# Kernel tuning notes

Hardware: AMD Instinct MI355X
Metric: run time of the kernel (lower is better)

The kernel has to match this reference:

```python
import jax, jax.numpy as jnp
import numpy as np

N_HEADS = 16


def setup_inputs() -> dict:
    key = jax.random.key(0)
    ks = jax.random.split(key, 5)
    E = 1024
    x = jax.random.normal(ks[0], (2, 2048, E), dtype=jnp.float32)
    s = 1.0 / np.sqrt(E)
    Wq = jax.random.normal(ks[1], (E, E), dtype=jnp.float32) * s
    Wk = jax.random.normal(ks[2], (E, E), dtype=jnp.float32) * s
    Wv = jax.random.normal(ks[3], (E, E), dtype=jnp.float32) * s
    Wo = jax.random.normal(ks[4], (E, E), dtype=jnp.float32) * s
    bo = jnp.zeros((E,), dtype=jnp.float32)
    return {"x": x, "Wq": Wq, "Wk": Wk, "Wv": Wv, "Wo": Wo, "bo": bo}


def reference(x, Wq, Wk, Wv, Wo, bo):
    B, S, E = x.shape
    H = N_HEADS
    D = E // H
    # project and split heads: [B, H, S, D]
    def split_heads(y):
        return y.reshape(B, S, H, D).transpose(0, 2, 1, 3)
    q = split_heads(x @ Wq)
    k = split_heads(x @ Wk)
    v = split_heads(x @ Wv)
    # full score matrix [B, H, S, S]
    scores = jnp.einsum('bhqd,bhkd->bhqk', q, k)
    causal = jnp.triu(jnp.ones((S, S), dtype=bool), k=1)
    scores = jnp.where(causal, -jnp.inf, scores)
    attn = jax.nn.softmax(scores / jnp.sqrt(jnp.float32(D)), axis=-1)
    # dropout rate is 0.0 -> identity
    ctx = jnp.einsum('bhqk,bhkd->bhqd', attn, v)
    ctx = ctx.transpose(0, 2, 1, 3).reshape(B, S, E)
    return ctx @ Wo + bo
```

## Files before the change

kernel.cpp:

```cpp
#include <hip/hip_runtime.h>
#include <stdint.h>


#define N_HEADS 16
#define HD 64
#define SEQ 2048
#define EMB 1024

typedef __attribute__((ext_vector_type(8))) short s16x8;
typedef __attribute__((ext_vector_type(4))) float f32x4;
typedef __attribute__((ext_vector_type(16))) float f32x16;

#define QSCALE 0.18033688f

template <bool B> struct BC { static constexpr bool value = B; };

__device__ __forceinline__ short f2b(float f) {
  union { float f; uint32_t u; } v; v.f = f;
  uint32_t u = v.u;
  u += 0x7fffu + ((u >> 16) & 1u);
  return (short)(u >> 16);
}

__device__ __forceinline__ uint32_t pk2(float a, float b) {
  union { float f; uint32_t u; } x, y; x.f = a; y.f = b;
  return ((x.u + 0x8000u) >> 16) | ((y.u + 0x8000u) & 0xffff0000u);
}

__device__ __forceinline__ float exp2a(float x) {
  float r; asm("v_exp_f32 %0, %1" : "=v"(r) : "v"(x)); return r;
}

__device__ __forceinline__ void gll16(const void* g, void* l) {
  __builtin_amdgcn_global_load_lds((const __attribute__((address_space(1))) void*)g,
                                   (__attribute__((address_space(3))) void*)l, 16, 0, 0);
}

#define SWZ(row, chunk) ((((row) * 8) + ((chunk) ^ ((row) & 7))) * 8)

__global__ __launch_bounds__(256) void k_prep(const float* __restrict__ x,
                                              const float* __restrict__ W0,
                                              const float* __restrict__ W1,
                                              const float* __restrict__ W2,
                                              const float* __restrict__ W3,
                                              short* __restrict__ xb,
                                              short* __restrict__ wt) {
  const int z = blockIdx.x, t = threadIdx.x;
  if (z < 4096) {
    int i = z * 256 + t;
    float4 v = ((const float4*)x)[i];
    short4 o;
    o.x = f2b(v.x); o.y = f2b(v.y); o.z = f2b(v.z); o.w = f2b(v.w);
    ((short4*)xb)[i] = o;
  } else {
    __shared__ float tile[32][33];
    int bz = z - 4096;
    int w = bz >> 10, rem = bz & 1023;
    int bn = (rem & 31) * 32, bk = (rem >> 5) * 32;
    const float* W = w == 0 ? W0 : w == 1 ? W1 : w == 2 ? W2 : W3;
    short* o = wt + (size_t)w * EMB * EMB;
    int tx = t & 31, ty = t >> 5;
    for (int i = ty; i < 32; i += 8)
      tile[i][tx] = W[(size_t)(bk + i) * EMB + bn + tx];
    __syncthreads();
    for (int i = ty; i < 32; i += 8)
      o[(size_t)(bn + i) * EMB + bk + tx] = f2b(tile[tx][i]);
  }
}

template <int MODE>
__global__ __launch_bounds__(256) void k_gemm(const short* __restrict__ A,
                                              const short* __restrict__ BT,
                                              void* __restrict__ outp,
                                              const float* __restrict__ bias) {
  constexpr int MAIN = 4 * 4096;
  constexpr int EPIL = (MODE == 1) ? 0 : 128 * 132;
  constexpr int SMSZ = MAIN > EPIL ? MAIN : EPIL;
  __shared__ alignas(16) short smem[SMSZ];

  const int t = threadIdx.x;
  const int by = blockIdx.y;
  const int m0 = blockIdx.x * 128;
  const short* Bp = BT + (size_t)by * (128 * EMB);
  const int wave = t >> 6, lane = t & 63;
  const int wm = (wave >> 1) * 64, wn = (wave & 1) * 64;
  const int l31 = lane & 31, lh = lane >> 5;

  const int srow = lane >> 2;
  const int soff = ((lane & 3) ^ (srow & 3)) * 8;

  auto stage = [&](int kb, int p) {
    short* as = smem + p * 4096;
    short* bs = smem + 8192 + p * 4096;
#pragma unroll
    for (int i = 0; i < 2; i++) {
      int rb = wave * 32 + i * 16;
      gll16(A + (size_t)(m0 + rb + srow) * EMB + kb + soff, &as[rb * 32]);
      gll16(Bp + (size_t)(rb + srow) * EMB + kb + soff, &bs[rb * 32]);
    }
  };
  auto frd = [&](const short* sb, int row, int kh) -> s16x8 {
    int c = kh * 2 + lh;
    return *(const s16x8*)&sb[row * 32 + ((c ^ (row & 3)) * 8)];
  };

  f32x16 acc[2][2] = {};

  auto kloop = [&](auto SWC) {
    constexpr bool SW = decltype(SWC)::value;
    int pb = 0;
    stage(0, 0);
    for (int kb = 0; kb < EMB; kb += 32) {
      __syncthreads();
      if (kb + 32 < EMB) stage(kb + 32, pb ^ 1);
      const short* as = smem + pb * 4096;
      const short* bs = smem + 8192 + pb * 4096;
      s16x8 af[2][2], bf[2][2];
#pragma unroll
      for (int mt = 0; mt < 2; mt++)
#pragma unroll
        for (int kh = 0; kh < 2; kh++) af[mt][kh] = frd(as, wm + mt * 32 + l31, kh);
#pragma unroll
      for (int nt = 0; nt < 2; nt++)
#pragma unroll
        for (int kh = 0; kh < 2; kh++) bf[nt][kh] = frd(bs, wn + nt * 32 + l31, kh);
#pragma unroll
      for (int mt = 0; mt < 2; mt++)
#pragma unroll
        for (int nt = 0; nt < 2; nt++)
#pragma unroll
          for (int kh = 0; kh < 2; kh++)
            acc[mt][nt] = SW
              ? __builtin_amdgcn_mfma_f32_32x32x16_bf16(bf[nt][kh], af[mt][kh], acc[mt][nt], 0, 0, 0)
              : __builtin_amdgcn_mfma_f32_32x32x16_bf16(af[mt][kh], bf[nt][kh], acc[mt][nt], 0, 0, 0);
      pb ^= 1;
    }
  };

  if (MODE == 1 || by < 16) kloop(BC<true>{});
  else                      kloop(BC<false>{});

  if (MODE == 0) {
    if (by < 16) {
      __syncthreads();
      short* Vls = smem;
      const int wsel = by >> 3;
      const float qs = (wsel == 0) ? QSCALE : 1.0f;
      const int n0l = (by & 7) * 128;
#pragma unroll
      for (int mt = 0; mt < 2; mt++) {
        int mr = wm + mt * 32 + l31;
#pragma unroll
        for (int nt = 0; nt < 2; nt++)
#pragma unroll
          for (int g = 0; g < 4; g++) {
            uint2 w;
            w.x = pk2(acc[mt][nt][4 * g + 0] * qs, acc[mt][nt][4 * g + 1] * qs);
            w.y = pk2(acc[mt][nt][4 * g + 2] * qs, acc[mt][nt][4 * g + 3] * qs);
            *(uint2*)&Vls[mr * 132 + wn + nt * 32 + g * 8 + 4 * lh] = w;
          }
      }
      __syncthreads();
      short* ob = (short*)outp + (size_t)wsel * (4u * 1024 * 1024);
      const int bb = m0 >> 11, ss0 = m0 & (SEQ - 1);
#pragma unroll
      for (int i = 0; i < 8; i++) {
        int mrow = i * 16 + (t >> 4);
        int ncol = (t & 15) * 8;
        int e = n0l + ncol, hh = e >> 6, dd = e & 63;
        *(uint4*)&ob[(((size_t)(bb * N_HEADS + hh) * SEQ) + ss0 + mrow) * 64 + dd] =
            *(const uint4*)&Vls[mrow * 132 + ncol];
      }
    } else {
      __syncthreads();
      short* Vls = smem;
#pragma unroll
      for (int nt = 0; nt < 2; nt++) {
        int nl = wn + nt * 32 + l31;
#pragma unroll
        for (int mt = 0; mt < 2; mt++)
#pragma unroll
          for (int g = 0; g < 4; g++) {
            uint2 w;
            w.x = pk2(acc[mt][nt][4 * g + 0], acc[mt][nt][4 * g + 1]);
            w.y = pk2(acc[mt][nt][4 * g + 2], acc[mt][nt][4 * g + 3]);
            *(uint2*)&Vls[nl * 132 + wm + mt * 32 + g * 8 + 4 * lh] = w;
          }
      }
      __syncthreads();
      short* obv = (short*)outp + (size_t)8 * 1024 * 1024;
      const int n0l = (by & 7) * 128;
      const int bb = m0 >> 11, ss0 = m0 & (SEQ - 1);
#pragma unroll
      for (int i = 0; i < 8; i++) {
        int nl = i * 16 + (t >> 4);
        int mc = (t & 15) * 8;
        int e = n0l + nl, hh = e >> 6, dd = e & 63;
        *(uint4*)&obv[((size_t)((bb * N_HEADS + hh) * HD + dd)) * SEQ + ss0 + mc] =
            *(const uint4*)&Vls[nl * 132 + mc];
      }
    }
  } else {
    float* of = (float*)outp;
    const int n0 = by * 128;
#pragma unroll
    for (int mt = 0; mt < 2; mt++) {
      int mg = m0 + wm + mt * 32 + l31;
#pragma unroll
      for (int nt = 0; nt < 2; nt++)
#pragma unroll
        for (int g = 0; g < 4; g++) {
          int ng = n0 + wn + nt * 32 + g * 8 + 4 * lh;
          f32x4 bv = *(const f32x4*)&bias[ng];
          f32x4 w;
          w[0] = acc[mt][nt][4 * g + 0] + bv[0];
          w[1] = acc[mt][nt][4 * g + 1] + bv[1];
          w[2] = acc[mt][nt][4 * g + 2] + bv[2];
          w[3] = acc[mt][nt][4 * g + 3] + bv[3];
          *(f32x4*)&of[(size_t)mg * EMB + ng] = w;
        }
    }
  }
}

__global__ __launch_bounds__(512) void k_attn(const short* __restrict__ Q,
                                              const short* __restrict__ K,
                                              const short* __restrict__ Vt,
                                              short* __restrict__ ctx) {
  __shared__ alignas(16) short UQP[128 * 72];
  __shared__ alignas(16) short Ks0[64 * 64], Ks1[64 * 64];
  __shared__ alignas(16) short Vs0[64 * 64], Vs1[64 * 64];

  const int t = threadIdx.x, wave = t >> 6, lane = t & 63;
  const int ml = lane & 15, quad = lane >> 4;
  const int bh = blockIdx.x;
  const int qb = 15 - (int)blockIdx.y;
  const size_t base = (size_t)bh * SEQ * HD;
  const int q0 = qb * 128, wq = q0 + wave * 16;

  const int sr = lane >> 3;
  const int sc = ((lane & 7) ^ sr) * 8;

#pragma unroll
  for (int i = 0; i < 2; i++) {
    int r8 = wave * 16 + i * 8;
    gll16(Q + base + (size_t)(q0 + r8 + sr) * HD + sc, &UQP[r8 * 64]);
  }
  auto stageKV = [&](int kt, short* kd, short* vd) {
    const int kbase = kt * 64;
    const int r8 = wave * 8;
    gll16(K + base + (size_t)(kbase + r8 + sr) * HD + sc, &kd[r8 * 64]);
    gll16(Vt + base + (size_t)(r8 + sr) * SEQ + kbase + sc, &vd[r8 * 64]);
  };

  f32x4 cacc[4] = {};
  float li = 0.f;
  short* Pw = &UQP[wave * 16 * 72];

  stageKV(0, Ks0, Vs0);
  __syncthreads();

  s16x8 qf[2];
#pragma unroll
  for (int c = 0; c < 2; c++)
    qf[c] = *(const s16x8*)&UQP[SWZ(wave * 16 + ml, 4 * c + quad)];
  __syncthreads();

  auto tile_body = [&](int kt, const short* kd, const short* vd) {
    const int kbase = kt * 64;
    if (kbase > wq + 15) return;
    const bool diag = (kbase + 63 > wq);
    f32x4 st[4];
#pragma unroll
    for (int nt = 0; nt < 4; nt++) {
      int row = nt * 16 + ml;
      s16x8 kf0 = *(const s16x8*)&kd[SWZ(row, quad)];
      s16x8 kf1 = *(const s16x8*)&kd[SWZ(row, 4 + quad)];
      f32x4 z = {};
      z = __builtin_amdgcn_mfma_f32_16x16x32_bf16(kf0, qf[0], z, 0, 0, 0);
      st[nt] = __builtin_amdgcn_mfma_f32_16x16x32_bf16(kf1, qf[1], z, 0, 0, 0);
    }
    const int qg = wq + ml;
    float rsum = 0.f;
#pragma unroll
    for (int nt = 0; nt < 4; nt++) {
      float p0 = exp2a(st[nt][0]);
      float p1 = exp2a(st[nt][1]);
      float p2 = exp2a(st[nt][2]);
      float p3 = exp2a(st[nt][3]);
      if (diag) {
        int kk = kbase + nt * 16 + quad * 4;
        if (kk + 0 > qg) p0 = 0.f;
        if (kk + 1 > qg) p1 = 0.f;
        if (kk + 2 > qg) p2 = 0.f;
        if (kk + 3 > qg) p3 = 0.f;
      }
      rsum += (p0 + p1) + (p2 + p3);
      uint2 w; w.x = pk2(p0, p1); w.y = pk2(p2, p3);
      *(uint2*)&Pw[ml * 72 + nt * 16 + quad * 4] = w;
    }
    li += rsum;
    __builtin_amdgcn_wave_barrier();

    s16x8 pf[2];
#pragma unroll
    for (int c = 0; c < 2; c++)
      pf[c] = *(const s16x8*)&Pw[ml * 72 + c * 32 + quad * 8];
#pragma unroll
    for (int mt = 0; mt < 4; mt++) {
      int row = mt * 16 + ml;
      s16x8 vf0 = *(const s16x8*)&vd[SWZ(row, quad)];
      s16x8 vf1 = *(const s16x8*)&vd[SWZ(row, 4 + quad)];
      cacc[mt] = __builtin_amdgcn_mfma_f32_16x16x32_bf16(vf0, pf[0], cacc[mt], 0, 0, 0);
      cacc[mt] = __builtin_amdgcn_mfma_f32_16x16x32_bf16(vf1, pf[1], cacc[mt], 0, 0, 0);
    }
  };

  const int nkt = 2 * qb + 2;
  for (int kt = 0; kt < nkt; kt += 2) {
    stageKV(kt + 1, Ks1, Vs1);
    tile_body(kt, Ks0, Vs0);
    __syncthreads();
    if (kt + 2 < nkt) stageKV(kt + 2, Ks0, Vs0);
    tile_body(kt + 1, Ks1, Vs1);
    __syncthreads();
  }

  li += __shfl_xor(li, 16, 64);
  li += __shfl_xor(li, 32, 64);
  float inv = 1.0f / li;
#pragma unroll
  for (int mt = 0; mt < 4; mt++) {
    uint2 w;
    w.x = pk2(cacc[mt][0] * inv, cacc[mt][1] * inv);
    w.y = pk2(cacc[mt][2] * inv, cacc[mt][3] * inv);
    *(uint2*)&Pw[ml * 72 + mt * 16 + quad * 4] = w;
  }
  __builtin_amdgcn_wave_barrier();
  const int b = bh >> 4, h = bh & 15;
#pragma unroll
  for (int i = 0; i < 2; i++) {
    int row = i * 8 + (lane >> 3);
    int q = wq + row;
    size_t gbase = ((size_t)(b * SEQ + q)) * EMB + h * 64 + (lane & 7) * 8;
    *(uint4*)&ctx[gbase] = *(const uint4*)&Pw[row * 72 + (lane & 7) * 8];
  }
}

extern "C" void kernel_launch(void* const* d_in, const int* in_sizes, int n_in,
                              void* d_out, int out_size, void* d_ws, size_t ws_size,
                              hipStream_t stream) {
  const float* x  = (const float*)d_in[0];
  const float* Wq = (const float*)d_in[1];
  const float* Wk = (const float*)d_in[2];
  const float* Wv = (const float*)d_in[3];
  const float* Wo = (const float*)d_in[4];
  const float* bo = (const float*)d_in[5];
  float* out = (float*)d_out;

  short* ws = (short*)d_ws;
  short* xb  = ws;
  short* wt  = ws + (size_t)4 * 1024 * 1024;
  short* qkv = ws + (size_t)8 * 1024 * 1024;

  k_prep<<<8192, 256, 0, stream>>>(x, Wq, Wk, Wv, Wo, xb, wt);
  k_gemm<0><<<dim3(32, 24), 256, 0, stream>>>(xb, wt, qkv, nullptr);
  k_attn<<<dim3(32, 16), 512, 0, stream>>>(qkv, qkv + (size_t)4 * 1024 * 1024,
                                           qkv + (size_t)8 * 1024 * 1024, xb);
  k_gemm<1><<<dim3(32, 8), 256, 0, stream>>>(xb, wt + (size_t)3 * 1024 * 1024, out, bo);
}
```

Measured before the change: 172.6 us.

## Switch attention to 32x32x16 MFMA with 4 waves of 32 query rows

The attention kernel now runs 256 threads per block, and each of its 4 waves owns 32 query rows. Both matmuls use the 32x32x16 bf16 MFMA instead of 16x16x32. Q fragments are loaded straight from global memory into registers rather than staged through LDS, and each wave stages twice the K/V rows. The query-block order is changed to interleave heavy and light causal blocks. The aim is fewer MFMA issues, fewer LDS fragment loads, and better load balance, at the cost of higher register pressure per wave and fewer waves per block.

```diff
diff --git a/kernel.cpp b/kernel.cpp
--- a/kernel.cpp
+++ b/kernel.cpp
@@ -223,97 +223,95 @@
   }
 }
 
-__global__ __launch_bounds__(512) void k_attn(const short* __restrict__ Q,
+__global__ __launch_bounds__(256) void k_attn(const short* __restrict__ Q,
                                               const short* __restrict__ K,
                                               const short* __restrict__ Vt,
                                               short* __restrict__ ctx) {
-  __shared__ alignas(16) short UQP[128 * 72];
+  __shared__ alignas(16) short Ps[4 * 32 * 72];
   __shared__ alignas(16) short Ks0[64 * 64], Ks1[64 * 64];
   __shared__ alignas(16) short Vs0[64 * 64], Vs1[64 * 64];
 
   const int t = threadIdx.x, wave = t >> 6, lane = t & 63;
-  const int ml = lane & 15, quad = lane >> 4;
+  const int l31 = lane & 31, lh = lane >> 5;
   const int bh = blockIdx.x;
-  const int qb = 15 - (int)blockIdx.y;
+  const int y = blockIdx.y;
+  const int qb = (y < 8) ? (15 - y) : (y - 8);
   const size_t base = (size_t)bh * SEQ * HD;
-  const int q0 = qb * 128, wq = q0 + wave * 16;
+  const int q0 = qb * 128, wq = q0 + wave * 32;
 
   const int sr = lane >> 3;
   const int sc = ((lane & 7) ^ sr) * 8;
 
-#pragma unroll
-  for (int i = 0; i < 2; i++) {
-    int r8 = wave * 16 + i * 8;
-    gll16(Q + base + (size_t)(q0 + r8 + sr) * HD + sc, &UQP[r8 * 64]);
-  }
+  s16x8 qf[4];
+#pragma unroll
+  for (int kh = 0; kh < 4; kh++)
+    qf[kh] = *(const s16x8*)(Q + base + (size_t)(wq + l31) * HD + kh * 16 + lh * 8);
+
   auto stageKV = [&](int kt, short* kd, short* vd) {
     const int kbase = kt * 64;
-    const int r8 = wave * 8;
-    gll16(K + base + (size_t)(kbase + r8 + sr) * HD + sc, &kd[r8 * 64]);
-    gll16(Vt + base + (size_t)(r8 + sr) * SEQ + kbase + sc, &vd[r8 * 64]);
-  };
-
-  f32x4 cacc[4] = {};
+#pragma unroll
+    for (int i = 0; i < 2; i++) {
+      int r8 = wave * 16 + i * 8;
+      gll16(K + base + (size_t)(kbase + r8 + sr) * HD + sc, &kd[r8 * 64]);
+      gll16(Vt + base + (size_t)(r8 + sr) * SEQ + kbase + sc, &vd[r8 * 64]);
+    }
+  };
+
+  f32x16 cacc[2] = {};
   float li = 0.f;
-  short* Pw = &UQP[wave * 16 * 72];
+  short* Pw = &Ps[wave * 32 * 72];
 
   stageKV(0, Ks0, Vs0);
   __syncthreads();
 
-  s16x8 qf[2];
-#pragma unroll
-  for (int c = 0; c < 2; c++)
-    qf[c] = *(const s16x8*)&UQP[SWZ(wave * 16 + ml, 4 * c + quad)];
-  __syncthreads();
-
   auto tile_body = [&](int kt, const short* kd, const short* vd) {
     const int kbase = kt * 64;
-    if (kbase > wq + 15) return;
+    if (kbase > wq + 31) return;
     const bool diag = (kbase + 63 > wq);
-    f32x4 st[4];
-#pragma unroll
-    for (int nt = 0; nt < 4; nt++) {
-      int row = nt * 16 + ml;
-      s16x8 kf0 = *(const s16x8*)&kd[SWZ(row, quad)];
-      s16x8 kf1 = *(const s16x8*)&kd[SWZ(row, 4 + quad)];
-      f32x4 z = {};
-      z = __builtin_amdgcn_mfma_f32_16x16x32_bf16(kf0, qf[0], z, 0, 0, 0);
-      st[nt] = __builtin_amdgcn_mfma_f32_16x16x32_bf16(kf1, qf[1], z, 0, 0, 0);
-    }
-    const int qg = wq + ml;
-    float rsum = 0.f;
-#pragma unroll
-    for (int nt = 0; nt < 4; nt++) {
-      float p0 = exp2a(st[nt][0]);
-      float p1 = exp2a(st[nt][1]);
-      float p2 = exp2a(st[nt][2]);
-      float p3 = exp2a(st[nt][3]);
-      if (diag) {
-        int kk = kbase + nt * 16 + quad * 4;
-        if (kk + 0 > qg) p0 = 0.f;
-        if (kk + 1 > qg) p1 = 0.f;
-        if (kk + 2 > qg) p2 = 0.f;
-        if (kk + 3 > qg) p3 = 0.f;
-      }
-      rsum += (p0 + p1) + (p2 + p3);
-      uint2 w; w.x = pk2(p0, p1); w.y = pk2(p2, p3);
-      *(uint2*)&Pw[ml * 72 + nt * 16 + quad * 4] = w;
-    }
-    li += rsum;
+    const int qg = wq + l31;
+#pragma unroll
+    for (int mt = 0; mt < 2; mt++) {
+      f32x16 st = {};
+#pragma unroll
+      for (int kh = 0; kh < 4; kh++) {
+        int c = 2 * kh + lh, row = mt * 32 + l31;
+        s16x8 kf = *(const s16x8*)&kd[SWZ(row, c)];
+        st = __builtin_amdgcn_mfma_f32_32x32x16_bf16(kf, qf[kh], st, 0, 0, 0);
+      }
+      float rsum = 0.f;
+#pragma unroll
+      for (int g = 0; g < 4; g++) {
+        float p0 = exp2a(st[4 * g + 0]);
+        float p1 = exp2a(st[4 * g + 1]);
+        float p2 = exp2a(st[4 * g + 2]);
+        float p3 = exp2a(st[4 * g + 3]);
+        if (diag) {
+          int kk = kbase + mt * 32 + 8 * g + 4 * lh;
+          if (kk + 0 > qg) p0 = 0.f;
+          if (kk + 1 > qg) p1 = 0.f;
+          if (kk + 2 > qg) p2 = 0.f;
+          if (kk + 3 > qg) p3 = 0.f;
+        }
+        rsum += (p0 + p1) + (p2 + p3);
+        uint2 w; w.x = pk2(p0, p1); w.y = pk2(p2, p3);
+        *(uint2*)&Pw[l31 * 72 + mt * 32 + g * 8 + 4 * lh] = w;
+      }
+      li += rsum;
+    }
     __builtin_amdgcn_wave_barrier();
 
-    s16x8 pf[2];
-#pragma unroll
-    for (int c = 0; c < 2; c++)
-      pf[c] = *(const s16x8*)&Pw[ml * 72 + c * 32 + quad * 8];
-#pragma unroll
-    for (int mt = 0; mt < 4; mt++) {
-      int row = mt * 16 + ml;
-      s16x8 vf0 = *(const s16x8*)&vd[SWZ(row, quad)];
-      s16x8 vf1 = *(const s16x8*)&vd[SWZ(row, 4 + quad)];
-      cacc[mt] = __builtin_amdgcn_mfma_f32_16x16x32_bf16(vf0, pf[0], cacc[mt], 0, 0, 0);
-      cacc[mt] = __builtin_amdgcn_mfma_f32_16x16x32_bf16(vf1, pf[1], cacc[mt], 0, 0, 0);
-    }
+    s16x8 pf[4];
+#pragma unroll
+    for (int kh = 0; kh < 4; kh++)
+      pf[kh] = *(const s16x8*)&Pw[l31 * 72 + kh * 16 + lh * 8];
+#pragma unroll
+    for (int mt = 0; mt < 2; mt++)
+#pragma unroll
+      for (int kh = 0; kh < 4; kh++) {
+        int c = 2 * kh + lh, row = mt * 32 + l31;
+        s16x8 vf = *(const s16x8*)&vd[SWZ(row, c)];
+        cacc[mt] = __builtin_amdgcn_mfma_f32_32x32x16_bf16(vf, pf[kh], cacc[mt], 0, 0, 0);
+      }
   };
 
   const int nkt = 2 * qb + 2;
@@ -326,20 +324,21 @@
     __syncthreads();
   }
 
-  li += __shfl_xor(li, 16, 64);
   li += __shfl_xor(li, 32, 64);
   float inv = 1.0f / li;
 #pragma unroll
-  for (int mt = 0; mt < 4; mt++) {
-    uint2 w;
-    w.x = pk2(cacc[mt][0] * inv, cacc[mt][1] * inv);
-    w.y = pk2(cacc[mt][2] * inv, cacc[mt][3] * inv);
-    *(uint2*)&Pw[ml * 72 + mt * 16 + quad * 4] = w;
-  }
+  for (int mt = 0; mt < 2; mt++)
+#pragma unroll
+    for (int g = 0; g < 4; g++) {
+      uint2 w;
+      w.x = pk2(cacc[mt][4 * g + 0] * inv, cacc[mt][4 * g + 1] * inv);
+      w.y = pk2(cacc[mt][4 * g + 2] * inv, cacc[mt][4 * g + 3] * inv);
+      *(uint2*)&Pw[l31 * 72 + mt * 32 + g * 8 + 4 * lh] = w;
+    }
   __builtin_amdgcn_wave_barrier();
   const int b = bh >> 4, h = bh & 15;
 #pragma unroll
-  for (int i = 0; i < 2; i++) {
+  for (int i = 0; i < 4; i++) {
     int row = i * 8 + (lane >> 3);
     int q = wq + row;
     size_t gbase = ((size_t)(b * SEQ + q)) * EMB + h * 64 + (lane & 7) * 8;
@@ -365,7 +364,7 @@
 
   k_prep<<<8192, 256, 0, stream>>>(x, Wq, Wk, Wv, Wo, xb, wt);
   k_gemm<0><<<dim3(32, 24), 256, 0, stream>>>(xb, wt, qkv, nullptr);
-  k_attn<<<dim3(32, 16), 512, 0, stream>>>(qkv, qkv + (size_t)4 * 1024 * 1024,
+  k_attn<<<dim3(32, 16), 256, 0, stream>>>(qkv, qkv + (size_t)4 * 1024 * 1024,
                                            qkv + (size_t)8 * 1024 * 1024, xb);
   k_gemm<1><<<dim3(32, 8), 256, 0, stream>>>(xb, wt + (size_t)3 * 1024 * 1024, out, bo);
 }
```

Result: slower. 177.6 us (+2.9%).
